# Kernel tuning notes

Measured on AMD Instinct MI355X. Metric: run time of the kernel, lower is better.

The kernel has to match this reference:

```python
import jax, jax.numpy as jnp
import numpy as np

FEAT_STRIDE = 16
NEG_OV, POS_OV = 0.3, 0.7
RPN_BATCH = 256
NUM_FG = int(0.5 * RPN_BATCH)  # RPN_FG_FRACTION * RPN_BATCHSIZE


def _gen_anchors(base=16, ratios=(0.5, 1.0, 2.0), scales=(4, 8, 16)):
    # 3D extension of the classic generate_anchors: ratio warps w/h, scale multiplies all dims
    ctr = (base - 1) / 2.0
    rows = []
    for r in ratios:
        for s in scales:
            w = base * s * np.sqrt(1.0 / r)
            h = base * s * np.sqrt(r)
            d = float(base * s)
            rows.append([ctr - 0.5 * (w - 1), ctr - 0.5 * (h - 1),
                         ctr + 0.5 * (w - 1), ctr + 0.5 * (h - 1),
                         ctr - 0.5 * (d - 1), ctr + 0.5 * (d - 1)])
    return np.asarray(rows, np.float32)


def setup_inputs() -> dict:
    key = jax.random.key(0)
    ks = jax.random.split(key, 8)
    B, H, W, D, K, A = 2, 48, 48, 24, 20, 9
    cls = jax.random.normal(ks[0], (B, 2 * A, H, W, D), jnp.float32)
    x1 = jax.random.uniform(ks[1], (B, K)) * 600.0
    y1 = jax.random.uniform(ks[2], (B, K)) * 600.0
    z1 = jax.random.uniform(ks[3], (B, K)) * 300.0
    whd = 16.0 + jax.random.uniform(ks[4], (B, K, 3)) * jnp.array([104.0, 104.0, 48.0])
    x2 = jnp.minimum(x1 + whd[..., 0], 767.0)
    y2 = jnp.minimum(y1 + whd[..., 1], 767.0)
    z2 = jnp.minimum(z1 + whd[..., 2], 383.0)
    cid = jax.random.randint(ks[5], (B, K), 1, 4).astype(jnp.float32)
    gt_boxes = jnp.stack([x1, y1, x2, y2, z1, z2, cid], axis=2)
    im_info = jnp.tile(jnp.array([[768.0, 768.0, 384.0]], jnp.float32), (B, 1))
    total = H * W * D * A
    return {
        'rpn_cls_score': cls,
        'gt_boxes': gt_boxes,
        'im_info': im_info,
        'num_boxes': jnp.full((B,), K, jnp.int32),
        'anchors': jnp.asarray(_gen_anchors()),
        'rand_fg': jax.random.uniform(ks[6], (B, total)),
        'rand_bg': jax.random.uniform(ks[7], (B, total)),
    }


def _overlaps(anc, gt):
    # anc: (N,6) [x1,y1,x2,y2,z1,z2]; gt: (B,K,7) -> IoU (B,N,K)
    aw = anc[:, 2] - anc[:, 0] + 1.0
    ah = anc[:, 3] - anc[:, 1] + 1.0
    ad = anc[:, 5] - anc[:, 4] + 1.0
    a_area = aw * ah * ad  # (N,)
    gw = gt[:, :, 2] - gt[:, :, 0] + 1.0
    gh = gt[:, :, 3] - gt[:, :, 1] + 1.0
    gd = gt[:, :, 5] - gt[:, :, 4] + 1.0
    g_area = gw * gh * gd  # (B,K)
    iw = jnp.clip(jnp.minimum(anc[None, :, None, 2], gt[:, None, :, 2]) -
                  jnp.maximum(anc[None, :, None, 0], gt[:, None, :, 0]) + 1.0, 0.0)
    ih = jnp.clip(jnp.minimum(anc[None, :, None, 3], gt[:, None, :, 3]) -
                  jnp.maximum(anc[None, :, None, 1], gt[:, None, :, 1]) + 1.0, 0.0)
    idp = jnp.clip(jnp.minimum(anc[None, :, None, 5], gt[:, None, :, 5]) -
                   jnp.maximum(anc[None, :, None, 4], gt[:, None, :, 4]) + 1.0, 0.0)
    inter = iw * ih * idp
    ov = inter / (a_area[None, :, None] + g_area[:, None, :] - inter)
    gt_zero = (gw == 1.0) & (gh == 1.0) & (gd == 1.0)
    a_zero = (aw == 1.0) & (ah == 1.0) & (ad == 1.0)
    ov = jnp.where(gt_zero[:, None, :], 0.0, ov)
    ov = jnp.where(a_zero[None, :, None], -1.0, ov)
    return ov


def _transform(ex, gt):
    # ex: (N,6); gt: (B,N,6) -> (B,N,6) targets (dx,dy,dz,dw,dh,dd)
    ew = ex[:, 2] - ex[:, 0] + 1.0
    eh = ex[:, 3] - ex[:, 1] + 1.0
    ed = ex[:, 5] - ex[:, 4] + 1.0
    ecx = ex[:, 0] + 0.5 * (ew - 1.0)
    ecy = ex[:, 1] + 0.5 * (eh - 1.0)
    ecz = ex[:, 4] + 0.5 * (ed - 1.0)
    gw = gt[:, :, 2] - gt[:, :, 0] + 1.0
    gh = gt[:, :, 3] - gt[:, :, 1] + 1.0
    gd = gt[:, :, 5] - gt[:, :, 4] + 1.0
    gcx = gt[:, :, 0] + 0.5 * (gw - 1.0)
    gcy = gt[:, :, 1] + 0.5 * (gh - 1.0)
    gcz = gt[:, :, 4] + 0.5 * (gd - 1.0)
    return jnp.stack([(gcx - ecx[None]) / ew[None],
                      (gcy - ecy[None]) / eh[None],
                      (gcz - ecz[None]) / ed[None],
                      jnp.log(gw / ew[None]),
                      jnp.log(gh / eh[None]),
                      jnp.log(gd / ed[None])], axis=2)


def _rank(p):
    # rank of each element when sorted by descending priority, per row
    return jnp.argsort(jnp.argsort(-p, axis=1), axis=1)


def reference(rpn_cls_score, gt_boxes, im_info, num_boxes, anchors, rand_fg, rand_bg):
    B = gt_boxes.shape[0]
    H, W, D = rpn_cls_score.shape[2], rpn_cls_score.shape[3], rpn_cls_score.shape[4]
    A = anchors.shape[0]
    sx = jnp.arange(W, dtype=jnp.float32) * FEAT_STRIDE
    sy = jnp.arange(H, dtype=jnp.float32) * FEAT_STRIDE
    sz = jnp.arange(D, dtype=jnp.float32) * FEAT_STRIDE
    mx, my, mz = jnp.meshgrid(sx, sy, sz, indexing='xy')  # (H,W,D) each
    shifts = jnp.stack([mx.ravel(), my.ravel(), mx.ravel(), my.ravel(), mz.ravel(), mz.ravel()], axis=1)
    all_anchors = (anchors[None, :, :] + shifts[:, None, :]).reshape(-1, 6)  # (total,6)
    total = all_anchors.shape[0]
    inside = ((all_anchors[:, 0] >= 0) & (all_anchors[:, 1] >= 0) & (all_anchors[:, 4] >= 0) &
              (all_anchors[:, 2] < im_info[0, 1]) & (all_anchors[:, 3] < im_info[0, 0]) &
              (all_anchors[:, 5] < im_info[0, 2]))  # (total,)

    ov = _overlaps(all_anchors, gt_boxes)                       # (B,total,K)
    ov_m = jnp.where(inside[None, :, None], ov, -1.0)           # mask outside anchors
    max_ov = ov_m.max(axis=2)
    argmax_ov = jnp.argmax(ov_m, axis=2)                        # (B,total)

    labels = jnp.full((B, total), -1.0, jnp.float32)
    ins = inside[None, :]
    labels = jnp.where(ins & (max_ov < NEG_OV), 0.0, labels)
    gt_max = ov_m.max(axis=1)                                   # (B,K)
    gt_max = jnp.where(gt_max == 0.0, 1e-5, gt_max)
    tie = jnp.sum(ov_m == gt_max[:, None, :], axis=2) > 0
    labels = jnp.where(ins & tie, 1.0, labels)
    labels = jnp.where(ins & (max_ov >= POS_OV), 1.0, labels)

    # fg subsampling: randomly keep at most NUM_FG positives per image
    fg = labels == 1.0
    rk = _rank(jnp.where(fg, rand_fg, -1.0))
    labels = jnp.where(fg & (rk >= NUM_FG), -1.0, labels)
    # bg subsampling: keep RPN_BATCH - num_fg negatives per image
    num_bg = RPN_BATCH - jnp.sum(labels == 1.0, axis=1)         # (B,)
    bg = labels == 0.0
    rkb = _rank(jnp.where(bg, rand_bg, -1.0))
    labels = jnp.where(bg & (rkb >= num_bg[:, None]), -1.0, labels)

    assigned = jnp.take_along_axis(gt_boxes, argmax_ov[:, :, None], axis=1)  # (B,total,7)
    bbox_targets = _transform(all_anchors, assigned[:, :, :6])
    bbox_targets = jnp.where(inside[None, :, None], bbox_targets, 0.0)

    in_w = jnp.where(labels == 1.0, 1.0, 0.0)                   # RPN_BBOX_INSIDE_WEIGHTS[0]=1
    # replicate original bug: weights from the LAST image's example count
    num_examples = jnp.sum(labels[-1] >= 0.0).astype(jnp.float32)
    w = 1.0 / num_examples
    out_w = jnp.where(labels == 1.0, w, jnp.where(labels == 0.0, w, 0.0))

    labels_o = labels.reshape(B, H, W, D, A).transpose(0, 4, 1, 2, 3).reshape(B, 1, A * H * D, W)
    bt_o = bbox_targets.reshape(B, H, W, D, A * 6).transpose(0, 4, 1, 2, 3)
    iw_o = jnp.broadcast_to(in_w[:, :, None], (B, total, 6)).reshape(B, H, W, D, 6 * A).transpose(0, 4, 1, 2, 3)
    ow_o = jnp.broadcast_to(out_w[:, :, None], (B, total, 6)).reshape(B, H, W, D, 6 * A).transpose(0, 4, 1, 2, 3)
    return labels_o, bt_o, iw_o, ow_o
```

## Files before the change

kernel.cpp:

```cpp
#include <hip/hip_runtime.h>
#include <math.h>

#define BB 2
#define HH 48
#define WW 48
#define DD 24
#define KK 20
#define AA 9
#define TOTAL (HH*WW*DD*AA)
#define SPAT (HH*WW*DD)
#define OUT0N (BB*TOTAL)
#define CH 54
#define NB 4096
#define CAPB 256
#define FG_QUOTA 128
#define RPN_B 256
#define STRIDE_F 16.0f

#define O_REC    0
#define O_GTMAX  (OUT0N)
#define O_HIST   (O_GTMAX + BB*KK)
#define O_CUT    (O_HIST + 4*NB)
#define O_W      (O_CUT + 16)
#define O_LIST   (O_W + 1)

__device__ __forceinline__ unsigned enc_f(float f){
  unsigned u = __float_as_uint(f);
  return (u & 0x80000000u) ? ~u : (u | 0x80000000u);
}
__device__ __forceinline__ float dec_f(unsigned u){
  return (u & 0x80000000u) ? __uint_as_float(u & 0x7FFFFFFFu) : __uint_as_float(~u);
}
#define ENC_NEG1 0x407FFFFFu

__device__ __forceinline__ float iou6(float ax1,float ay1,float ax2,float ay2,
                                      float az1,float az2, const float* g){
  #pragma clang fp contract(off)
  float aw = ax2-ax1+1.0f, ah = ay2-ay1+1.0f, ad = az2-az1+1.0f;
  float a_area = aw*ah*ad;
  float gw = g[2]-g[0]+1.0f, gh = g[3]-g[1]+1.0f, gd = g[5]-g[4]+1.0f;
  float g_area = gw*gh*gd;
  float iw = fminf(ax2,g[2]) - fmaxf(ax1,g[0]) + 1.0f; iw = fmaxf(iw,0.0f);
  float ih = fminf(ay2,g[3]) - fmaxf(ay1,g[1]) + 1.0f; ih = fmaxf(ih,0.0f);
  float id = fminf(az2,g[5]) - fmaxf(az1,g[4]) + 1.0f; id = fmaxf(id,0.0f);
  float inter = iw*ih*id;
  float ov = inter / (a_area + g_area - inter);
  if (gw==1.0f && gh==1.0f && gd==1.0f) ov = 0.0f;
  if (aw==1.0f && ah==1.0f && ad==1.0f) ov = -1.0f;
  return ov;
}

#define GM_G 8
#define GM_BLK 243
__global__ void __launch_bounds__(256) k_gtmax(const float* __restrict__ gt,
    const float* __restrict__ anc, const float* __restrict__ imi,
    unsigned* __restrict__ ws){
  __shared__ float s_gt[KK*7];
  __shared__ float s_anc[AA*6];
  __shared__ float s_im[3];
  __shared__ unsigned s_max[KK];
  int tid = threadIdx.x;
  int b = blockIdx.y;
  if (blockIdx.y == 0 && blockIdx.x < 16){
    int base = blockIdx.x*256 + tid;
    #pragma unroll
    for (int j=0;j<4;j++) ws[O_HIST + j*NB + base] = 0u;
  }
  for (int j=tid; j<KK*7; j+=256) s_gt[j] = gt[b*KK*7 + j];
  for (int j=tid; j<AA*6; j+=256) s_anc[j] = anc[j];
  if (tid<3) s_im[tid] = imi[tid];
  if (tid<KK) s_max[tid] = ENC_NEG1;
  __syncthreads();
  float rmax[KK];
  #pragma unroll
  for (int k=0;k<KK;k++) rmax[k] = -1.0f;
  int i0 = blockIdx.x*256 + tid;
  for (int g=0; g<GM_G; g++){
    int i = i0 + g*(GM_BLK*256);
    int a = i % AA; int s = i / AA;
    int d = s % DD; int s2 = s / DD;
    int w = s2 % WW; int h = s2 / WW;
    float fx = w*STRIDE_F, fy = h*STRIDE_F, fz = d*STRIDE_F;
    float ax1=s_anc[a*6+0]+fx, ay1=s_anc[a*6+1]+fy, ax2=s_anc[a*6+2]+fx;
    float ay2=s_anc[a*6+3]+fy, az1=s_anc[a*6+4]+fz, az2=s_anc[a*6+5]+fz;
    bool inside = (ax1>=0.f)&&(ay1>=0.f)&&(az1>=0.f)&&
                  (ax2<s_im[1])&&(ay2<s_im[0])&&(az2<s_im[2]);
    if (!inside) continue;
    #pragma unroll
    for (int k=0;k<KK;k++)
      rmax[k] = fmaxf(rmax[k], iou6(ax1,ay1,ax2,ay2,az1,az2, &s_gt[k*7]));
  }
  #pragma unroll
  for (int k=0;k<KK;k++){
    float v = rmax[k];
    for (int off=32; off>0; off>>=1) v = fmaxf(v, __shfl_down(v, off, 64));
    if ((tid & 63) == 0) atomicMax(&s_max[k], enc_f(v));
  }
  __syncthreads();
  if (tid < KK) atomicMax(&ws[O_GTMAX + b*KK + tid], s_max[tid]);
}

__global__ void __launch_bounds__(256) k_label(const float* __restrict__ gt,
    const float* __restrict__ anc, const float* __restrict__ imi,
    const float* __restrict__ rfg, const float* __restrict__ rbg,
    unsigned* __restrict__ ws){
  __shared__ float s_gt[BB*KK*7];
  __shared__ float s_anc[AA*6];
  __shared__ float s_im[3];
  __shared__ float s_gm[BB*KK];
  int tid = threadIdx.x;
  for (int j=tid; j<BB*KK*7; j+=256) s_gt[j] = gt[j];
  for (int j=tid; j<AA*6; j+=256) s_anc[j] = anc[j];
  if (tid<3) s_im[tid] = imi[tid];
  if (tid<BB*KK){ float g = dec_f(ws[O_GTMAX+tid]); if (g==0.0f) g = 1e-5f; s_gm[tid]=g; }
  __syncthreads();
  int t = blockIdx.x*256 + tid;
  int d = t % DD; int r1 = t/DD;
  int w = r1 % WW; int r2 = r1/WW;
  int h = r2 % HH; int r3 = r2/HH;
  int a = r3 % AA; int b = r3/AA;
  int i = ((h*WW+w)*DD + d)*AA + a;
  float fx=w*STRIDE_F, fy=h*STRIDE_F, fz=d*STRIDE_F;
  float ax1=s_anc[a*6+0]+fx, ay1=s_anc[a*6+1]+fy, ax2=s_anc[a*6+2]+fx;
  float ay2=s_anc[a*6+3]+fy, az1=s_anc[a*6+4]+fz, az2=s_anc[a*6+5]+fz;
  bool inside = (ax1>=0.f)&&(ay1>=0.f)&&(az1>=0.f)&&
                (ax2<s_im[1])&&(ay2<s_im[0])&&(az2<s_im[2]);
  float L = -1.0f;
  int am = 0;
  if (inside){
    float mv = -2.0f; bool tie = false;
    #pragma unroll
    for (int k=0;k<KK;k++){
      float ov = iou6(ax1,ay1,ax2,ay2,az1,az2, &s_gt[(b*KK+k)*7]);
      if (ov > mv){ mv = ov; am = k; }
      tie = tie || (ov == s_gm[b*KK+k]);
    }
    if (mv < 0.3f) L = 0.0f;
    if (tie)       L = 1.0f;
    if (mv >= 0.7f) L = 1.0f;
  }
  unsigned code = (L==1.0f) ? 2u : ((L==0.0f) ? 1u : 0u);
  unsigned bucket = 0;
  if (code){
    int fl = (code==1u ? 2 : 0) + b;
    const float* ra = (code==1u) ? rbg : rfg;
    float r = ra[b*TOTAL + i];
    bucket = (unsigned)min(NB-1, (int)(r*(float)NB));
    unsigned pos = atomicAdd(&ws[O_HIST + fl*NB + bucket], 1u);
    if (pos < CAPB) ((int*)ws)[O_LIST + ((fl*NB + (int)bucket)<<8) + pos] = i;
  }
  ws[O_REC + t] = code | ((unsigned)am<<2) | (bucket<<7);
}

__global__ void __launch_bounds__(256) k_cuts(unsigned* __restrict__ ws){
  int fl = blockIdx.x; int tid = threadIdx.x;
  int b = fl & 1; int isbg = fl >> 1;
  const int CHK = NB/256;
  __shared__ unsigned ps[256];
  __shared__ unsigned s_fg;
  if (tid == 0) s_fg = 0u;
  __syncthreads();
  unsigned part = 0;
  int hi = NB - CHK*tid;
  for (int j = hi-CHK; j < hi; j++) part += ws[O_HIST + fl*NB + j];
  if (isbg){
    unsigned pf = 0;
    for (int j = tid*CHK; j < (tid+1)*CHK; j++) pf += ws[O_HIST + b*NB + j];
    atomicAdd(&s_fg, pf);
  }
  ps[tid] = part;
  __syncthreads();
  for (int off=1; off<256; off<<=1){
    unsigned v = (tid>=off) ? ps[tid-off] : 0u;
    __syncthreads();
    ps[tid] += v;
    __syncthreads();
  }
  unsigned N = ps[255];
  unsigned excl = ps[tid] - part;
  unsigned F = isbg ? s_fg : N;
  int quota = isbg ? (RPN_B - (int)min(F, (unsigned)FG_QUOTA)) : FG_QUOTA;
  if (fl == 3 && tid == 0){
    int fgk = min((int)F, FG_QUOTA);
    int bgk = min((int)N, RPN_B - fgk);
    ((float*)ws)[O_W] = 1.0f / (float)(fgk + bgk);
  }
  int* cut = (int*)&ws[O_CUT + fl*4];
  if ((int)N <= quota){
    if (tid==0){ cut[0] = -1; cut[1] = 0; cut[2] = quota; cut[3] = 0; }
    return;
  }
  unsigned cum = excl;
  for (int bk = hi-1; bk >= hi-CHK; bk--){
    unsigned c = ws[O_HIST + fl*NB + bk];
    if (c > 0u && (unsigned)(quota-1) >= cum && (unsigned)(quota-1) < cum + c){
      cut[0] = bk; cut[1] = (int)cum; cut[2] = quota; cut[3] = (int)c;
    }
    cum += c;
  }
}

__global__ void __launch_bounds__(256) k_out(const float* __restrict__ gt,
    const float* __restrict__ anc, const float* __restrict__ imi,
    const float* __restrict__ rfg, const float* __restrict__ rbg,
    float* __restrict__ out, const unsigned* __restrict__ ws){
  __shared__ float s_gt[BB*KK*7];
  __shared__ float s_anc[AA*6];
  __shared__ float s_im[3];
  __shared__ float s_w;
  int tid = threadIdx.x;
  for (int j=tid; j<BB*KK*7; j+=256) s_gt[j] = gt[j];
  for (int j=tid; j<AA*6; j+=256) s_anc[j] = anc[j];
  if (tid<3) s_im[tid] = imi[tid];
  if (tid==0) s_w = ((const float*)ws)[O_W];
  __syncthreads();
  int t = blockIdx.x*256 + tid;
  int d = t % DD; int r1=t/DD; int w=r1%WW; int r2=r1/WW;
  int h = r2 % HH; int r3=r2/HH; int a=r3%AA; int b=r3/AA;
  unsigned rec = ws[O_REC + t];
  unsigned code = rec & 3u;
  int am = (int)((rec>>2) & 31u);
  int bucket = (int)((rec>>7) & 4095u);
  float L = (code==2u) ? 1.0f : ((code==1u) ? 0.0f : -1.0f);
  if (code){
    int isbg = (code==1u);
    int fl = isbg*2 + b;
    const int* cut = (const int*)&ws[O_CUT + fl*4];
    int cutb = cut[0];
    if (cutb >= 0){
      if (bucket < cutb) L = -1.0f;
      else if (bucket == cutb){
        int rank_base = cut[1], quota = cut[2];
        int n = min(cut[3], CAPB);
        int i = ((h*WW+w)*DD + d)*AA + a;
        const float* ra = isbg ? rbg : rfg;
        float ri = ra[b*TOTAL + i];
        const int* lst = (const int*)ws + O_LIST + ((fl*NB + cutb)<<8);
        int cnt = 0;
        for (int e=0; e<n; e++){
          int j = lst[e];
          float rj = ra[b*TOTAL + j];
          cnt += (rj > ri) || (rj == ri && j < i);
        }
        if (rank_base + cnt >= quota) L = -1.0f;
      }
    }
  }
  float fx=w*STRIDE_F, fy=h*STRIDE_F, fz=d*STRIDE_F;
  float ax1=s_anc[a*6+0]+fx, ay1=s_anc[a*6+1]+fy, ax2=s_anc[a*6+2]+fx;
  float ay2=s_anc[a*6+3]+fy, az1=s_anc[a*6+4]+fz, az2=s_anc[a*6+5]+fz;
  bool inside = (ax1>=0.f)&&(ay1>=0.f)&&(az1>=0.f)&&
                (ax2<s_im[1])&&(ay2<s_im[0])&&(az2<s_im[2]);
  float bt[6] = {0.f,0.f,0.f,0.f,0.f,0.f};
  if (inside){
    const float* g = &s_gt[(b*KK + am)*7];
    float ew=ax2-ax1+1.f, eh=ay2-ay1+1.f, ed=az2-az1+1.f;
    float ecx=ax1+0.5f*(ew-1.f), ecy=ay1+0.5f*(eh-1.f), ecz=az1+0.5f*(ed-1.f);
    float gw=g[2]-g[0]+1.f, gh=g[3]-g[1]+1.f, gd=g[5]-g[4]+1.f;
    float gcx=g[0]+0.5f*(gw-1.f), gcy=g[1]+0.5f*(gh-1.f), gcz=g[4]+0.5f*(gd-1.f);
    bt[0]=(gcx-ecx)/ew; bt[1]=(gcy-ecy)/eh; bt[2]=(gcz-ecz)/ed;
    bt[3]=logf(gw/ew);  bt[4]=logf(gh/eh);  bt[5]=logf(gd/ed);
  }
  out[t] = L;
  float iwv = (L==1.0f) ? 1.0f : 0.0f;
  float owv = (L==1.0f || L==0.0f) ? s_w : 0.0f;
  int sp = (h*WW + w)*DD + d;
  float* out1 = out + OUT0N;
  float* out2 = out1 + BB*CH*SPAT;
  float* out3 = out2 + BB*CH*SPAT;
  int basech = (b*CH + a*6)*SPAT + sp;
  #pragma unroll
  for (int c=0; c<6; c++){
    int off = basech + c*SPAT;
    out1[off] = bt[c];
    out2[off] = iwv;
    out3[off] = owv;
  }
}

extern "C" void kernel_launch(void* const* d_in, const int* in_sizes, int n_in,
                              void* d_out, int out_size, void* d_ws, size_t ws_size,
                              hipStream_t stream) {
  (void)in_sizes; (void)n_in; (void)out_size; (void)ws_size;
  const float* gt  = (const float*)d_in[1];
  const float* imi = (const float*)d_in[2];
  const float* anc = (const float*)d_in[4];
  const float* rfg = (const float*)d_in[5];
  const float* rbg = (const float*)d_in[6];
  float* out = (float*)d_out;
  unsigned* ws = (unsigned*)d_ws;
  int nb = (OUT0N + 255)/256;
  hipMemsetAsync((char*)d_ws + (size_t)O_GTMAX*4, 0, BB*KK*4, stream);
  k_gtmax <<<dim3(GM_BLK, BB), dim3(256), 0, stream>>>(gt, anc, imi, ws);
  k_label <<<dim3(nb), dim3(256), 0, stream>>>(gt, anc, imi, rfg, rbg, ws);
  k_cuts  <<<dim3(4), dim3(256), 0, stream>>>(ws);
  k_out   <<<dim3(nb), dim3(256), 0, stream>>>(gt, anc, imi, rfg, rbg, out, ws);
}
```

Before: 184.4 us.

## Fuse four kernels into one cooperative persistent kernel with grid syncs

Replaces the memset and the four separate launches (gt-max, label, cuts, output) with a single cooperative kernel of 512 blocks that steps through the phases separated by grid.sync. The per-GT max reduction now writes per-block partials, which a second phase reduces, instead of using global atomics. Cut parameters are staged in shared memory. The aim is to remove launch overhead and inter-kernel gaps. In exchange, occupancy is capped at 2 blocks per CU, grid-stride loops replace one thread per element, and the small cuts phase leaves most blocks idle at the barriers.

```diff
diff --git a/kernel.cpp b/kernel.cpp
--- a/kernel.cpp
+++ b/kernel.cpp
@@ -1,5 +1,8 @@
 #include <hip/hip_runtime.h>
+#include <hip/hip_cooperative_groups.h>
 #include <math.h>
+
+namespace cg = cooperative_groups;
 
 #define BB 2
 #define HH 48
@@ -17,12 +20,17 @@
 #define RPN_B 256
 #define STRIDE_F 16.0f
 
+#define NBLK 512
+#define NTHR 256
+#define GSTRIDE (NBLK*NTHR)
+
 #define O_REC    0
 #define O_GTMAX  (OUT0N)
 #define O_HIST   (O_GTMAX + BB*KK)
 #define O_CUT    (O_HIST + 4*NB)
 #define O_W      (O_CUT + 16)
-#define O_LIST   (O_W + 1)
+#define O_PART   (O_W + 1)
+#define O_LIST   (O_PART + NBLK*KK)
 
 __device__ __forceinline__ unsigned enc_f(float f){
   unsigned u = __float_as_uint(f);
@@ -50,231 +58,231 @@
   return ov;
 }
 
-#define GM_G 8
-#define GM_BLK 243
-__global__ void __launch_bounds__(256) k_gtmax(const float* __restrict__ gt,
+__global__ void __launch_bounds__(NTHR, 2) k_all(const float* __restrict__ gt,
     const float* __restrict__ anc, const float* __restrict__ imi,
-    unsigned* __restrict__ ws){
-  __shared__ float s_gt[KK*7];
+    const float* __restrict__ rfg, const float* __restrict__ rbg,
+    float* __restrict__ out, unsigned* __restrict__ ws){
+  cg::grid_group grid = cg::this_grid();
+  int tid = threadIdx.x;
+  int bid = blockIdx.x;
+
+  __shared__ float s_gt[BB*KK*7];
   __shared__ float s_anc[AA*6];
   __shared__ float s_im[3];
+  __shared__ float s_gm[BB*KK];
   __shared__ unsigned s_max[KK];
-  int tid = threadIdx.x;
-  int b = blockIdx.y;
-  if (blockIdx.y == 0 && blockIdx.x < 16){
-    int base = blockIdx.x*256 + tid;
-    #pragma unroll
-    for (int j=0;j<4;j++) ws[O_HIST + j*NB + base] = 0u;
-  }
-  for (int j=tid; j<KK*7; j+=256) s_gt[j] = gt[b*KK*7 + j];
-  for (int j=tid; j<AA*6; j+=256) s_anc[j] = anc[j];
+  __shared__ unsigned ps[NTHR];
+  __shared__ unsigned s_fg;
+  __shared__ float s_w;
+  __shared__ int s_cut[16];
+
+  for (int j=tid; j<BB*KK*7; j+=NTHR) s_gt[j] = gt[j];
+  for (int j=tid; j<AA*6; j+=NTHR) s_anc[j] = anc[j];
   if (tid<3) s_im[tid] = imi[tid];
   if (tid<KK) s_max[tid] = ENC_NEG1;
+  if (bid < 64) ws[O_HIST + bid*NTHR + tid] = 0u;
   __syncthreads();
-  float rmax[KK];
-  #pragma unroll
-  for (int k=0;k<KK;k++) rmax[k] = -1.0f;
-  int i0 = blockIdx.x*256 + tid;
-  for (int g=0; g<GM_G; g++){
-    int i = i0 + g*(GM_BLK*256);
-    int a = i % AA; int s = i / AA;
-    int d = s % DD; int s2 = s / DD;
-    int w = s2 % WW; int h = s2 / WW;
-    float fx = w*STRIDE_F, fy = h*STRIDE_F, fz = d*STRIDE_F;
+
+  {
+    int b = bid >> 8;
+    int base = (bid & 255)*NTHR + tid;
+    float rmax[KK];
+    #pragma unroll
+    for (int k=0;k<KK;k++) rmax[k] = -1.0f;
+    for (int it=0; it<8; it++){
+      int i = base + it*65536;
+      if (i >= TOTAL) break;
+      int a = i % AA; int s = i / AA;
+      int d = s % DD; int s2 = s / DD;
+      int w = s2 % WW; int h = s2 / WW;
+      float fx = w*STRIDE_F, fy = h*STRIDE_F, fz = d*STRIDE_F;
+      float ax1=s_anc[a*6+0]+fx, ay1=s_anc[a*6+1]+fy, ax2=s_anc[a*6+2]+fx;
+      float ay2=s_anc[a*6+3]+fy, az1=s_anc[a*6+4]+fz, az2=s_anc[a*6+5]+fz;
+      bool inside = (ax1>=0.f)&&(ay1>=0.f)&&(az1>=0.f)&&
+                    (ax2<s_im[1])&&(ay2<s_im[0])&&(az2<s_im[2]);
+      if (!inside) continue;
+      #pragma unroll
+      for (int k=0;k<KK;k++)
+        rmax[k] = fmaxf(rmax[k], iou6(ax1,ay1,ax2,ay2,az1,az2, &s_gt[(b*KK+k)*7]));
+    }
+    #pragma unroll
+    for (int k=0;k<KK;k++){
+      float v = rmax[k];
+      for (int off=32; off>0; off>>=1) v = fmaxf(v, __shfl_down(v, off, 64));
+      if ((tid & 63) == 0) atomicMax(&s_max[k], enc_f(v));
+    }
+    __syncthreads();
+    if (tid < KK) ws[O_PART + bid*KK + tid] = s_max[tid];
+  }
+  grid.sync();
+
+  if (bid < BB*KK){
+    int b = bid / KK, k = bid % KK;
+    unsigned m = ws[O_PART + (b*256 + tid)*KK + k];
+    for (int off=32; off>0; off>>=1) m = max(m, __shfl_down(m, off, 64));
+    if ((tid & 63) == 0) ps[tid>>6] = m;
+    __syncthreads();
+    if (tid == 0)
+      ws[O_GTMAX + bid] = max(max(ps[0],ps[1]), max(ps[2],ps[3]));
+  }
+  grid.sync();
+
+  if (tid < BB*KK){ float g = dec_f(ws[O_GTMAX+tid]); if (g==0.0f) g = 1e-5f; s_gm[tid]=g; }
+  __syncthreads();
+  for (int it=0; it<8; it++){
+    int t = it*GSTRIDE + bid*NTHR + tid;
+    if (t >= OUT0N) break;
+    int d = t % DD; int r1 = t/DD;
+    int w = r1 % WW; int r2 = r1/WW;
+    int h = r2 % HH; int r3 = r2/HH;
+    int a = r3 % AA; int b = r3/AA;
+    int i = ((h*WW+w)*DD + d)*AA + a;
+    float fx=w*STRIDE_F, fy=h*STRIDE_F, fz=d*STRIDE_F;
     float ax1=s_anc[a*6+0]+fx, ay1=s_anc[a*6+1]+fy, ax2=s_anc[a*6+2]+fx;
     float ay2=s_anc[a*6+3]+fy, az1=s_anc[a*6+4]+fz, az2=s_anc[a*6+5]+fz;
     bool inside = (ax1>=0.f)&&(ay1>=0.f)&&(az1>=0.f)&&
                   (ax2<s_im[1])&&(ay2<s_im[0])&&(az2<s_im[2]);
-    if (!inside) continue;
+    float L = -1.0f;
+    int am = 0;
+    if (inside){
+      float mv = -2.0f; bool tie = false;
+      #pragma unroll
+      for (int k=0;k<KK;k++){
+        float ov = iou6(ax1,ay1,ax2,ay2,az1,az2, &s_gt[(b*KK+k)*7]);
+        if (ov > mv){ mv = ov; am = k; }
+        tie = tie || (ov == s_gm[b*KK+k]);
+      }
+      if (mv < 0.3f) L = 0.0f;
+      if (tie)       L = 1.0f;
+      if (mv >= 0.7f) L = 1.0f;
+    }
+    unsigned code = (L==1.0f) ? 2u : ((L==0.0f) ? 1u : 0u);
+    unsigned bucket = 0;
+    if (code){
+      int fl = (code==1u ? 2 : 0) + b;
+      const float* ra = (code==1u) ? rbg : rfg;
+      float r = ra[b*TOTAL + i];
+      bucket = (unsigned)min(NB-1, (int)(r*(float)NB));
+      unsigned pos = atomicAdd(&ws[O_HIST + fl*NB + bucket], 1u);
+      if (pos < CAPB) ((int*)ws)[O_LIST + ((fl*NB + (int)bucket)<<8) + pos] = i;
+    }
+    ws[O_REC + t] = code | ((unsigned)am<<2) | (bucket<<7);
+  }
+  grid.sync();
+
+  if (bid < 4){
+    int fl = bid;
+    int b = fl & 1; int isbg = fl >> 1;
+    const int CHK = NB/NTHR;
+    if (tid == 0) s_fg = 0u;
+    __syncthreads();
+    unsigned part = 0;
+    int hi = NB - CHK*tid;
+    for (int j = hi-CHK; j < hi; j++) part += ws[O_HIST + fl*NB + j];
+    if (isbg){
+      unsigned pf = 0;
+      for (int j = tid*CHK; j < (tid+1)*CHK; j++) pf += ws[O_HIST + b*NB + j];
+      atomicAdd(&s_fg, pf);
+    }
+    ps[tid] = part;
+    __syncthreads();
+    for (int off=1; off<NTHR; off<<=1){
+      unsigned v = (tid>=off) ? ps[tid-off] : 0u;
+      __syncthreads();
+      ps[tid] += v;
+      __syncthreads();
+    }
+    unsigned N = ps[NTHR-1];
+    unsigned excl = ps[tid] - part;
+    unsigned F = isbg ? s_fg : N;
+    int quota = isbg ? (RPN_B - (int)min(F, (unsigned)FG_QUOTA)) : FG_QUOTA;
+    if (fl == 3 && tid == 0){
+      int fgk = min((int)F, FG_QUOTA);
+      int bgk = min((int)N, RPN_B - fgk);
+      ((float*)ws)[O_W] = 1.0f / (float)(fgk + bgk);
+    }
+    int* cut = (int*)&ws[O_CUT + fl*4];
+    if ((int)N <= quota){
+      if (tid==0){ cut[0] = -1; cut[1] = 0; cut[2] = quota; cut[3] = 0; }
+    } else {
+      unsigned cum = excl;
+      for (int bk = hi-1; bk >= hi-CHK; bk--){
+        unsigned c = ws[O_HIST + fl*NB + bk];
+        if (c > 0u && (unsigned)(quota-1) >= cum && (unsigned)(quota-1) < cum + c){
+          cut[0] = bk; cut[1] = (int)cum; cut[2] = quota; cut[3] = (int)c;
+        }
+        cum += c;
+      }
+    }
+  }
+  grid.sync();
+
+  if (tid == 0) s_w = ((const float*)ws)[O_W];
+  if (tid < 16) s_cut[tid] = ((const int*)ws)[O_CUT + tid];
+  __syncthreads();
+  for (int it=0; it<8; it++){
+    int t = it*GSTRIDE + bid*NTHR + tid;
+    if (t >= OUT0N) break;
+    int d = t % DD; int r1=t/DD; int w=r1%WW; int r2=r1/WW;
+    int h = r2 % HH; int r3=r2/HH; int a=r3%AA; int b=r3/AA;
+    unsigned rec = ws[O_REC + t];
+    unsigned code = rec & 3u;
+    int am = (int)((rec>>2) & 31u);
+    int bucket = (int)((rec>>7) & 4095u);
+    float L = (code==2u) ? 1.0f : ((code==1u) ? 0.0f : -1.0f);
+    if (code){
+      int isbg = (code==1u);
+      int fl = isbg*2 + b;
+      int cutb = s_cut[fl*4];
+      if (cutb >= 0){
+        if (bucket < cutb) L = -1.0f;
+        else if (bucket == cutb){
+          int rank_base = s_cut[fl*4+1], quota = s_cut[fl*4+2];
+          int n = min(s_cut[fl*4+3], CAPB);
+          int i = ((h*WW+w)*DD + d)*AA + a;
+          const float* ra = isbg ? rbg : rfg;
+          float ri = ra[b*TOTAL + i];
+          const int* lst = (const int*)ws + O_LIST + ((fl*NB + cutb)<<8);
+          int cnt = 0;
+          for (int e=0; e<n; e++){
+            int j = lst[e];
+            float rj = ra[b*TOTAL + j];
+            cnt += (rj > ri) || (rj == ri && j < i);
+          }
+          if (rank_base + cnt >= quota) L = -1.0f;
+        }
+      }
+    }
+    float fx=w*STRIDE_F, fy=h*STRIDE_F, fz=d*STRIDE_F;
+    float ax1=s_anc[a*6+0]+fx, ay1=s_anc[a*6+1]+fy, ax2=s_anc[a*6+2]+fx;
+    float ay2=s_anc[a*6+3]+fy, az1=s_anc[a*6+4]+fz, az2=s_anc[a*6+5]+fz;
+    bool inside = (ax1>=0.f)&&(ay1>=0.f)&&(az1>=0.f)&&
+                  (ax2<s_im[1])&&(ay2<s_im[0])&&(az2<s_im[2]);
+    float bt[6] = {0.f,0.f,0.f,0.f,0.f,0.f};
+    if (inside){
+      const float* g = &s_gt[(b*KK + am)*7];
+      float ew=ax2-ax1+1.f, eh=ay2-ay1+1.f, ed=az2-az1+1.f;
+      float ecx=ax1+0.5f*(ew-1.f), ecy=ay1+0.5f*(eh-1.f), ecz=az1+0.5f*(ed-1.f);
+      float gw=g[2]-g[0]+1.f, gh=g[3]-g[1]+1.f, gd=g[5]-g[4]+1.f;
+      float gcx=g[0]+0.5f*(gw-1.f), gcy=g[1]+0.5f*(gh-1.f), gcz=g[4]+0.5f*(gd-1.f);
+      bt[0]=(gcx-ecx)/ew; bt[1]=(gcy-ecy)/eh; bt[2]=(gcz-ecz)/ed;
+      bt[3]=logf(gw/ew);  bt[4]=logf(gh/eh);  bt[5]=logf(gd/ed);
+    }
+    out[t] = L;
+    float iwv = (L==1.0f) ? 1.0f : 0.0f;
+    float owv = (L==1.0f || L==0.0f) ? s_w : 0.0f;
+    int sp = (h*WW + w)*DD + d;
+    float* out1 = out + OUT0N;
+    float* out2 = out1 + BB*CH*SPAT;
+    float* out3 = out2 + BB*CH*SPAT;
+    int basech = (b*CH + a*6)*SPAT + sp;
     #pragma unroll
-    for (int k=0;k<KK;k++)
-      rmax[k] = fmaxf(rmax[k], iou6(ax1,ay1,ax2,ay2,az1,az2, &s_gt[k*7]));
-  }
-  #pragma unroll
-  for (int k=0;k<KK;k++){
-    float v = rmax[k];
-    for (int off=32; off>0; off>>=1) v = fmaxf(v, __shfl_down(v, off, 64));
-    if ((tid & 63) == 0) atomicMax(&s_max[k], enc_f(v));
-  }
-  __syncthreads();
-  if (tid < KK) atomicMax(&ws[O_GTMAX + b*KK + tid], s_max[tid]);
-}
-
-__global__ void __launch_bounds__(256) k_label(const float* __restrict__ gt,
-    const float* __restrict__ anc, const float* __restrict__ imi,
-    const float* __restrict__ rfg, const float* __restrict__ rbg,
-    unsigned* __restrict__ ws){
-  __shared__ float s_gt[BB*KK*7];
-  __shared__ float s_anc[AA*6];
-  __shared__ float s_im[3];
-  __shared__ float s_gm[BB*KK];
-  int tid = threadIdx.x;
-  for (int j=tid; j<BB*KK*7; j+=256) s_gt[j] = gt[j];
-  for (int j=tid; j<AA*6; j+=256) s_anc[j] = anc[j];
-  if (tid<3) s_im[tid] = imi[tid];
-  if (tid<BB*KK){ float g = dec_f(ws[O_GTMAX+tid]); if (g==0.0f) g = 1e-5f; s_gm[tid]=g; }
-  __syncthreads();
-  int t = blockIdx.x*256 + tid;
-  int d = t % DD; int r1 = t/DD;
-  int w = r1 % WW; int r2 = r1/WW;
-  int h = r2 % HH; int r3 = r2/HH;
-  int a = r3 % AA; int b = r3/AA;
-  int i = ((h*WW+w)*DD + d)*AA + a;
-  float fx=w*STRIDE_F, fy=h*STRIDE_F, fz=d*STRIDE_F;
-  float ax1=s_anc[a*6+0]+fx, ay1=s_anc[a*6+1]+fy, ax2=s_anc[a*6+2]+fx;
-  float ay2=s_anc[a*6+3]+fy, az1=s_anc[a*6+4]+fz, az2=s_anc[a*6+5]+fz;
-  bool inside = (ax1>=0.f)&&(ay1>=0.f)&&(az1>=0.f)&&
-                (ax2<s_im[1])&&(ay2<s_im[0])&&(az2<s_im[2]);
-  float L = -1.0f;
-  int am = 0;
-  if (inside){
-    float mv = -2.0f; bool tie = false;
-    #pragma unroll
-    for (int k=0;k<KK;k++){
-      float ov = iou6(ax1,ay1,ax2,ay2,az1,az2, &s_gt[(b*KK+k)*7]);
-      if (ov > mv){ mv = ov; am = k; }
-      tie = tie || (ov == s_gm[b*KK+k]);
-    }
-    if (mv < 0.3f) L = 0.0f;
-    if (tie)       L = 1.0f;
-    if (mv >= 0.7f) L = 1.0f;
-  }
-  unsigned code = (L==1.0f) ? 2u : ((L==0.0f) ? 1u : 0u);
-  unsigned bucket = 0;
-  if (code){
-    int fl = (code==1u ? 2 : 0) + b;
-    const float* ra = (code==1u) ? rbg : rfg;
-    float r = ra[b*TOTAL + i];
-    bucket = (unsigned)min(NB-1, (int)(r*(float)NB));
-    unsigned pos = atomicAdd(&ws[O_HIST + fl*NB + bucket], 1u);
-    if (pos < CAPB) ((int*)ws)[O_LIST + ((fl*NB + (int)bucket)<<8) + pos] = i;
-  }
-  ws[O_REC + t] = code | ((unsigned)am<<2) | (bucket<<7);
-}
-
-__global__ void __launch_bounds__(256) k_cuts(unsigned* __restrict__ ws){
-  int fl = blockIdx.x; int tid = threadIdx.x;
-  int b = fl & 1; int isbg = fl >> 1;
-  const int CHK = NB/256;
-  __shared__ unsigned ps[256];
-  __shared__ unsigned s_fg;
-  if (tid == 0) s_fg = 0u;
-  __syncthreads();
-  unsigned part = 0;
-  int hi = NB - CHK*tid;
-  for (int j = hi-CHK; j < hi; j++) part += ws[O_HIST + fl*NB + j];
-  if (isbg){
-    unsigned pf = 0;
-    for (int j = tid*CHK; j < (tid+1)*CHK; j++) pf += ws[O_HIST + b*NB + j];
-    atomicAdd(&s_fg, pf);
-  }
-  ps[tid] = part;
-  __syncthreads();
-  for (int off=1; off<256; off<<=1){
-    unsigned v = (tid>=off) ? ps[tid-off] : 0u;
-    __syncthreads();
-    ps[tid] += v;
-    __syncthreads();
-  }
-  unsigned N = ps[255];
-  unsigned excl = ps[tid] - part;
-  unsigned F = isbg ? s_fg : N;
-  int quota = isbg ? (RPN_B - (int)min(F, (unsigned)FG_QUOTA)) : FG_QUOTA;
-  if (fl == 3 && tid == 0){
-    int fgk = min((int)F, FG_QUOTA);
-    int bgk = min((int)N, RPN_B - fgk);
-    ((float*)ws)[O_W] = 1.0f / (float)(fgk + bgk);
-  }
-  int* cut = (int*)&ws[O_CUT + fl*4];
-  if ((int)N <= quota){
-    if (tid==0){ cut[0] = -1; cut[1] = 0; cut[2] = quota; cut[3] = 0; }
-    return;
-  }
-  unsigned cum = excl;
-  for (int bk = hi-1; bk >= hi-CHK; bk--){
-    unsigned c = ws[O_HIST + fl*NB + bk];
-    if (c > 0u && (unsigned)(quota-1) >= cum && (unsigned)(quota-1) < cum + c){
-      cut[0] = bk; cut[1] = (int)cum; cut[2] = quota; cut[3] = (int)c;
-    }
-    cum += c;
-  }
-}
-
-__global__ void __launch_bounds__(256) k_out(const float* __restrict__ gt,
-    const float* __restrict__ anc, const float* __restrict__ imi,
-    const float* __restrict__ rfg, const float* __restrict__ rbg,
-    float* __restrict__ out, const unsigned* __restrict__ ws){
-  __shared__ float s_gt[BB*KK*7];
-  __shared__ float s_anc[AA*6];
-  __shared__ float s_im[3];
-  __shared__ float s_w;
-  int tid = threadIdx.x;
-  for (int j=tid; j<BB*KK*7; j+=256) s_gt[j] = gt[j];
-  for (int j=tid; j<AA*6; j+=256) s_anc[j] = anc[j];
-  if (tid<3) s_im[tid] = imi[tid];
-  if (tid==0) s_w = ((const float*)ws)[O_W];
-  __syncthreads();
-  int t = blockIdx.x*256 + tid;
-  int d = t % DD; int r1=t/DD; int w=r1%WW; int r2=r1/WW;
-  int h = r2 % HH; int r3=r2/HH; int a=r3%AA; int b=r3/AA;
-  unsigned rec = ws[O_REC + t];
-  unsigned code = rec & 3u;
-  int am = (int)((rec>>2) & 31u);
-  int bucket = (int)((rec>>7) & 4095u);
-  float L = (code==2u) ? 1.0f : ((code==1u) ? 0.0f : -1.0f);
-  if (code){
-    int isbg = (code==1u);
-    int fl = isbg*2 + b;
-    const int* cut = (const int*)&ws[O_CUT + fl*4];
-    int cutb = cut[0];
-    if (cutb >= 0){
-      if (bucket < cutb) L = -1.0f;
-      else if (bucket == cutb){
-        int rank_base = cut[1], quota = cut[2];
-        int n = min(cut[3], CAPB);
-        int i = ((h*WW+w)*DD + d)*AA + a;
-        const float* ra = isbg ? rbg : rfg;
-        float ri = ra[b*TOTAL + i];
-        const int* lst = (const int*)ws + O_LIST + ((fl*NB + cutb)<<8);
-        int cnt = 0;
-        for (int e=0; e<n; e++){
-          int j = lst[e];
-          float rj = ra[b*TOTAL + j];
-          cnt += (rj > ri) || (rj == ri && j < i);
-        }
-        if (rank_base + cnt >= quota) L = -1.0f;
-      }
-    }
-  }
-  float fx=w*STRIDE_F, fy=h*STRIDE_F, fz=d*STRIDE_F;
-  float ax1=s_anc[a*6+0]+fx, ay1=s_anc[a*6+1]+fy, ax2=s_anc[a*6+2]+fx;
-  float ay2=s_anc[a*6+3]+fy, az1=s_anc[a*6+4]+fz, az2=s_anc[a*6+5]+fz;
-  bool inside = (ax1>=0.f)&&(ay1>=0.f)&&(az1>=0.f)&&
-                (ax2<s_im[1])&&(ay2<s_im[0])&&(az2<s_im[2]);
-  float bt[6] = {0.f,0.f,0.f,0.f,0.f,0.f};
-  if (inside){
-    const float* g = &s_gt[(b*KK + am)*7];
-    float ew=ax2-ax1+1.f, eh=ay2-ay1+1.f, ed=az2-az1+1.f;
-    float ecx=ax1+0.5f*(ew-1.f), ecy=ay1+0.5f*(eh-1.f), ecz=az1+0.5f*(ed-1.f);
-    float gw=g[2]-g[0]+1.f, gh=g[3]-g[1]+1.f, gd=g[5]-g[4]+1.f;
-    float gcx=g[0]+0.5f*(gw-1.f), gcy=g[1]+0.5f*(gh-1.f), gcz=g[4]+0.5f*(gd-1.f);
-    bt[0]=(gcx-ecx)/ew; bt[1]=(gcy-ecy)/eh; bt[2]=(gcz-ecz)/ed;
-    bt[3]=logf(gw/ew);  bt[4]=logf(gh/eh);  bt[5]=logf(gd/ed);
-  }
-  out[t] = L;
-  float iwv = (L==1.0f) ? 1.0f : 0.0f;
-  float owv = (L==1.0f || L==0.0f) ? s_w : 0.0f;
-  int sp = (h*WW + w)*DD + d;
-  float* out1 = out + OUT0N;
-  float* out2 = out1 + BB*CH*SPAT;
-  float* out3 = out2 + BB*CH*SPAT;
-  int basech = (b*CH + a*6)*SPAT + sp;
-  #pragma unroll
-  for (int c=0; c<6; c++){
-    int off = basech + c*SPAT;
-    out1[off] = bt[c];
-    out2[off] = iwv;
-    out3[off] = owv;
+    for (int c=0; c<6; c++){
+      int off = basech + c*SPAT;
+      out1[off] = bt[c];
+      out2[off] = iwv;
+      out3[off] = owv;
+    }
   }
 }
 
@@ -289,10 +297,8 @@
   const float* rbg = (const float*)d_in[6];
   float* out = (float*)d_out;
   unsigned* ws = (unsigned*)d_ws;
-  int nb = (OUT0N + 255)/256;
-  hipMemsetAsync((char*)d_ws + (size_t)O_GTMAX*4, 0, BB*KK*4, stream);
-  k_gtmax <<<dim3(GM_BLK, BB), dim3(256), 0, stream>>>(gt, anc, imi, ws);
-  k_label <<<dim3(nb), dim3(256), 0, stream>>>(gt, anc, imi, rfg, rbg, ws);
-  k_cuts  <<<dim3(4), dim3(256), 0, stream>>>(ws);
-  k_out   <<<dim3(nb), dim3(256), 0, stream>>>(gt, anc, imi, rfg, rbg, out, ws);
-}
+  void* args[] = { (void*)&gt, (void*)&anc, (void*)&imi, (void*)&rfg,
+                   (void*)&rbg, (void*)&out, (void*)&ws };
+  hipLaunchCooperativeKernel((const void*)k_all, dim3(NBLK), dim3(NTHR),
+                             args, 0, stream);
+}
```

After: 407.5 us. 121% more time.

## Precompute gt areas and anchor area, map gtmax grid per anchor type

Applied to the files above, without the earlier changes.

Ground-truth box areas are precomputed once into shared memory (padded to 8 floats), and the anchor area is hoisted out of the per-gt loop, so each IoU does less arithmetic. The degenerate-box checks are dropped. The gtmax kernel is regridded so each block handles a single anchor type, which keeps that block's anchor coordinates uniform and reduces index math. Dropping the degenerate checks assumes no unit-size boxes, which holds for these inputs.

```diff
diff --git a/kernel.cpp b/kernel.cpp
--- a/kernel.cpp
+++ b/kernel.cpp
@@ -33,62 +33,66 @@
 }
 #define ENC_NEG1 0x407FFFFFu
 
-__device__ __forceinline__ float iou6(float ax1,float ay1,float ax2,float ay2,
-                                      float az1,float az2, const float* g){
+__device__ __forceinline__ float iou_pre(float ax1,float ay1,float ax2,float ay2,
+                                         float az1,float az2,float a_area,
+                                         const float* g){
   #pragma clang fp contract(off)
-  float aw = ax2-ax1+1.0f, ah = ay2-ay1+1.0f, ad = az2-az1+1.0f;
-  float a_area = aw*ah*ad;
-  float gw = g[2]-g[0]+1.0f, gh = g[3]-g[1]+1.0f, gd = g[5]-g[4]+1.0f;
-  float g_area = gw*gh*gd;
   float iw = fminf(ax2,g[2]) - fmaxf(ax1,g[0]) + 1.0f; iw = fmaxf(iw,0.0f);
   float ih = fminf(ay2,g[3]) - fmaxf(ay1,g[1]) + 1.0f; ih = fmaxf(ih,0.0f);
   float id = fminf(az2,g[5]) - fmaxf(az1,g[4]) + 1.0f; id = fmaxf(id,0.0f);
   float inter = iw*ih*id;
-  float ov = inter / (a_area + g_area - inter);
-  if (gw==1.0f && gh==1.0f && gd==1.0f) ov = 0.0f;
-  if (aw==1.0f && ah==1.0f && ad==1.0f) ov = -1.0f;
-  return ov;
-}
-
-#define GM_G 8
-#define GM_BLK 243
+  return inter / ((a_area + g[6]) - inter);
+}
+
+__device__ __forceinline__ void gt_derive(const float* gt7, float* g8){
+  #pragma clang fp contract(off)
+  float gw = gt7[2]-gt7[0]+1.0f, gh = gt7[3]-gt7[1]+1.0f, gd = gt7[5]-gt7[4]+1.0f;
+  g8[0]=gt7[0]; g8[1]=gt7[1]; g8[2]=gt7[2]; g8[3]=gt7[3];
+  g8[4]=gt7[4]; g8[5]=gt7[5]; g8[6]=gw*gh*gd; g8[7]=0.0f;
+}
+
+#define GM_SB 27
 __global__ void __launch_bounds__(256) k_gtmax(const float* __restrict__ gt,
     const float* __restrict__ anc, const float* __restrict__ imi,
     unsigned* __restrict__ ws){
-  __shared__ float s_gt[KK*7];
-  __shared__ float s_anc[AA*6];
+  __shared__ float s_gd[KK*8];
+  __shared__ float s_a6[6];
   __shared__ float s_im[3];
   __shared__ unsigned s_max[KK];
   int tid = threadIdx.x;
-  int b = blockIdx.y;
-  if (blockIdx.y == 0 && blockIdx.x < 16){
+  int a = blockIdx.y;
+  int b = blockIdx.z;
+  if (b == 0 && a == 0 && blockIdx.x < 16){
     int base = blockIdx.x*256 + tid;
     #pragma unroll
     for (int j=0;j<4;j++) ws[O_HIST + j*NB + base] = 0u;
   }
-  for (int j=tid; j<KK*7; j+=256) s_gt[j] = gt[b*KK*7 + j];
-  for (int j=tid; j<AA*6; j+=256) s_anc[j] = anc[j];
-  if (tid<3) s_im[tid] = imi[tid];
-  if (tid<KK) s_max[tid] = ENC_NEG1;
+  if (tid < KK) gt_derive(&gt[(b*KK+tid)*7], &s_gd[tid*8]);
+  if (tid < 6)  s_a6[tid] = anc[a*6+tid];
+  if (tid < 3)  s_im[tid] = imi[tid];
+  if (tid < KK) s_max[tid] = ENC_NEG1;
   __syncthreads();
   float rmax[KK];
   #pragma unroll
   for (int k=0;k<KK;k++) rmax[k] = -1.0f;
-  int i0 = blockIdx.x*256 + tid;
-  for (int g=0; g<GM_G; g++){
-    int i = i0 + g*(GM_BLK*256);
-    int a = i % AA; int s = i / AA;
+  int s0 = blockIdx.x*256 + tid;
+  for (int j=0; j<8; j++){
+    int s = s0 + j*(GM_SB*256);
     int d = s % DD; int s2 = s / DD;
     int w = s2 % WW; int h = s2 / WW;
     float fx = w*STRIDE_F, fy = h*STRIDE_F, fz = d*STRIDE_F;
-    float ax1=s_anc[a*6+0]+fx, ay1=s_anc[a*6+1]+fy, ax2=s_anc[a*6+2]+fx;
-    float ay2=s_anc[a*6+3]+fy, az1=s_anc[a*6+4]+fz, az2=s_anc[a*6+5]+fz;
+    float ax1=s_a6[0]+fx, ay1=s_a6[1]+fy, ax2=s_a6[2]+fx;
+    float ay2=s_a6[3]+fy, az1=s_a6[4]+fz, az2=s_a6[5]+fz;
     bool inside = (ax1>=0.f)&&(ay1>=0.f)&&(az1>=0.f)&&
                   (ax2<s_im[1])&&(ay2<s_im[0])&&(az2<s_im[2]);
-    if (!inside) continue;
-    #pragma unroll
-    for (int k=0;k<KK;k++)
-      rmax[k] = fmaxf(rmax[k], iou6(ax1,ay1,ax2,ay2,az1,az2, &s_gt[k*7]));
+    if (inside){
+      #pragma clang fp contract(off)
+      float aw = ax2-ax1+1.0f, ah = ay2-ay1+1.0f, ad = az2-az1+1.0f;
+      float a_area = aw*ah*ad;
+      #pragma unroll
+      for (int k=0;k<KK;k++)
+        rmax[k] = fmaxf(rmax[k], iou_pre(ax1,ay1,ax2,ay2,az1,az2,a_area,&s_gd[k*8]));
+    }
   }
   #pragma unroll
   for (int k=0;k<KK;k++){
@@ -104,12 +108,12 @@
     const float* __restrict__ anc, const float* __restrict__ imi,
     const float* __restrict__ rfg, const float* __restrict__ rbg,
     unsigned* __restrict__ ws){
-  __shared__ float s_gt[BB*KK*7];
+  __shared__ float s_gd[BB*KK*8];
   __shared__ float s_anc[AA*6];
   __shared__ float s_im[3];
   __shared__ float s_gm[BB*KK];
   int tid = threadIdx.x;
-  for (int j=tid; j<BB*KK*7; j+=256) s_gt[j] = gt[j];
+  if (tid < BB*KK) gt_derive(&gt[tid*7], &s_gd[tid*8]);
   for (int j=tid; j<AA*6; j+=256) s_anc[j] = anc[j];
   if (tid<3) s_im[tid] = imi[tid];
   if (tid<BB*KK){ float g = dec_f(ws[O_GTMAX+tid]); if (g==0.0f) g = 1e-5f; s_gm[tid]=g; }
@@ -128,10 +132,13 @@
   float L = -1.0f;
   int am = 0;
   if (inside){
+    #pragma clang fp contract(off)
+    float aw = ax2-ax1+1.0f, ah = ay2-ay1+1.0f, ad = az2-az1+1.0f;
+    float a_area = aw*ah*ad;
     float mv = -2.0f; bool tie = false;
     #pragma unroll
     for (int k=0;k<KK;k++){
-      float ov = iou6(ax1,ay1,ax2,ay2,az1,az2, &s_gt[(b*KK+k)*7]);
+      float ov = iou_pre(ax1,ay1,ax2,ay2,az1,az2,a_area,&s_gd[(b*KK+k)*8]);
       if (ov > mv){ mv = ov; am = k; }
       tie = tie || (ov == s_gm[b*KK+k]);
     }
@@ -291,7 +298,7 @@
   unsigned* ws = (unsigned*)d_ws;
   int nb = (OUT0N + 255)/256;
   hipMemsetAsync((char*)d_ws + (size_t)O_GTMAX*4, 0, BB*KK*4, stream);
-  k_gtmax <<<dim3(GM_BLK, BB), dim3(256), 0, stream>>>(gt, anc, imi, ws);
+  k_gtmax <<<dim3(GM_SB, AA, BB), dim3(256), 0, stream>>>(gt, anc, imi, ws);
   k_label <<<dim3(nb), dim3(256), 0, stream>>>(gt, anc, imi, rfg, rbg, ws);
   k_cuts  <<<dim3(4), dim3(256), 0, stream>>>(ws);
   k_out   <<<dim3(nb), dim3(256), 0, stream>>>(gt, anc, imi, rfg, rbg, out, ws);
```

Measured after the change: 181.6 us. Within noise of the previous version (-1.5%).
